# Kernel tuning notes

Measured on AMD Instinct MI355X. Metric: run time of the kernel, lower is better.

The kernel has to match this reference:

```python
import jax, jax.numpy as jnp
import numpy as np

B, F, NQ, DT, TS, K = 16384, 256, 2048, 256, 16, 8
GH, SH, CALH = 128, 128, 16
SPD = DT + TS
SPH = max(int(SPD * 0.25), 16)
CD = DT + 3 + TS + 3  # h_base + y_base + 3 gate stats + z_top + |d_safe| + |d_spec| = 278
CH = max(int(CD * 0.25), 16)
RES_SCALE = 0.1


def _ln(x, g, b):
    m = x.mean(-1, keepdims=True)
    v = ((x - m) ** 2).mean(-1, keepdims=True)
    return (x - m) * jax.lax.rsqrt(v + 1e-5) * g + b


def _resmlp(x, lg, lb, w1, b1, w2, b2):
    h = jnp.maximum(_ln(x, lg, lb) @ w1 + b1, 0.0)
    return h @ w2 + b2


def setup_inputs() -> dict:
    key = jax.random.key(0)
    ks = iter(jax.random.split(key, 48))
    def nrm(shape, s=0.05):
        return jax.random.normal(next(ks), shape, jnp.float32) * s
    d = {}
    d["x_num"] = jax.random.normal(next(ks), (B, F), jnp.float32)
    d["robust_center"] = nrm((1, F), 0.1)
    d["robust_scale"] = jax.random.uniform(next(ks), (1, F), jnp.float32, 0.5, 1.5)
    d["quantile_sorted"] = jnp.sort(jax.random.normal(next(ks), (NQ, F), jnp.float32), axis=0)
    d["stem_w1"] = nrm((3, CALH)); d["stem_b1"] = jnp.zeros((CALH,))
    d["stem_w2"] = nrm((CALH, CALH)); d["stem_b2"] = jnp.zeros((CALH,))
    d["stem_w3"] = nrm((CALH, 1)); d["stem_b3"] = jnp.zeros((1,))
    d["gate_w1"] = nrm((F, GH)); d["gate_b1"] = jnp.zeros((GH,))
    d["gate_w2"] = nrm((GH, F)); d["gate_b2"] = jnp.zeros((F,))
    d["bb_w"] = nrm((F, DT)); d["bb_b"] = jnp.zeros((DT,))
    d["base_w"] = nrm((DT, 1)); d["base_b"] = jnp.zeros((1,))
    d["safe_lg"] = jnp.ones((DT,)); d["safe_lb"] = jnp.zeros((DT,))
    d["safe_w1"] = nrm((DT, SH)); d["safe_b1"] = jnp.zeros((SH,))
    d["safe_w2"] = nrm((SH, 1)); d["safe_b2"] = jnp.zeros((1,))
    d["top_w1"] = nrm((1, TS)); d["top_b1"] = jnp.zeros((TS,))
    d["top_w2"] = nrm((TS, TS)); d["top_b2"] = jnp.zeros((TS,))
    d["spec_lg"] = jnp.ones((SPD,)); d["spec_lb"] = jnp.zeros((SPD,))
    d["spec_w1"] = nrm((SPD, SPH)); d["spec_b1"] = jnp.zeros((SPH,))
    d["spec_w2"] = nrm((SPH, 1)); d["spec_b2"] = jnp.zeros((1,))
    d["conf_lg"] = jnp.ones((CD,)); d["conf_lb"] = jnp.zeros((CD,))
    d["conf_w1"] = nrm((CD, CH)); d["conf_b1"] = jnp.zeros((CH,))
    d["conf_w2"] = nrm((CH, 1)); d["conf_b2"] = jnp.full((1,), -2.0)  # gamma_init_bias
    return d


def _forward(x_num, robust_center, robust_scale, quantile_sorted,
             stem_w1, stem_b1, stem_w2, stem_b2, stem_w3, stem_b3,
             gate_w1, gate_b1, gate_w2, gate_b2,
             bb_w, bb_b, base_w, base_b,
             safe_lg, safe_lb, safe_w1, safe_b1, safe_w2, safe_b2,
             top_w1, top_b1, top_w2, top_b2,
             spec_lg, spec_lb, spec_w1, spec_b1, spec_w2, spec_b2,
             conf_lg, conf_lb, conf_w1, conf_b1, conf_w2, conf_b2):
    # --- calibration views ---
    x_robust = (x_num - robust_center) / robust_scale
    ranks = jax.vmap(jnp.searchsorted, in_axes=(1, 1), out_axes=1)(
        jax.lax.stop_gradient(quantile_sorted), jax.lax.stop_gradient(x_num))  # [B,F] int
    x_quant = jnp.clip(ranks.astype(jnp.float32) / (NQ - 1.0), 0.0, 1.0)
    x_views = jnp.stack([x_num, x_robust, x_quant], axis=-1)  # [B,F,3]
    h = jnp.maximum(x_views @ stem_w1 + stem_b1, 0.0)
    h = jnp.maximum(h @ stem_w2 + stem_b2, 0.0)
    resid = jnp.tanh((h @ stem_w3 + stem_b3)[..., 0])
    x_cal = x_num + RES_SCALE * resid
    # --- input gate ---
    g = jax.nn.sigmoid(jnp.maximum(x_cal @ gate_w1 + gate_b1, 0.0) @ gate_w2 + gate_b2)
    x_gated = x_cal * g
    # --- backbone (stand-in for TMLPBackbone.encode_hidden) ---
    h_base = jnp.maximum(x_gated @ bb_w + bb_b, 0.0)  # [B,DT]
    y_base = h_base @ base_w + base_b  # [B,1]
    gate_mean = g.mean(axis=1, keepdims=True)
    gate_max = g.max(axis=1, keepdims=True)
    gate_std = g.std(axis=1, keepdims=True)  # ddof=0, matches unbiased=False
    delta_safe = _resmlp(h_base, safe_lg, safe_lb, safe_w1, safe_b1, safe_w2, safe_b2)
    # --- top-k feature gather ---
    topk_g, topk_idx = jax.lax.top_k(g, K)
    topk_x = jnp.take_along_axis(x_cal, topk_idx, axis=1)
    topk_w = topk_g / (topk_g.sum(axis=1, keepdims=True) + 1e-6)
    xw = (topk_x * topk_w)[..., None]  # [B,K,1]
    tok = jnp.maximum(xw @ top_w1 + top_b1, 0.0) @ top_w2 + top_b2  # [B,K,TS]
    z_top = tok.mean(axis=1)  # [B,TS]
    delta_spec = _resmlp(jnp.concatenate([h_base, z_top], axis=1),
                         spec_lg, spec_lb, spec_w1, spec_b1, spec_w2, spec_b2)
    conf_in = jnp.concatenate([h_base, y_base, gate_mean, gate_max, gate_std,
                               z_top, jnp.abs(delta_safe), jnp.abs(delta_spec)], axis=1)
    gamma = jax.nn.sigmoid(_resmlp(conf_in, conf_lg, conf_lb, conf_w1, conf_b1, conf_w2, conf_b2))
    return (y_base + delta_safe + gamma * delta_spec)[:, 0]


def reference(x_num, robust_center, robust_scale, quantile_sorted,
              stem_w1, stem_b1, stem_w2, stem_b2, stem_w3, stem_b3,
              gate_w1, gate_b1, gate_w2, gate_b2,
              bb_w, bb_b, base_w, base_b,
              safe_lg, safe_lb, safe_w1, safe_b1, safe_w2, safe_b2,
              top_w1, top_b1, top_w2, top_b2,
              spec_lg, spec_lb, spec_w1, spec_b1, spec_w2, spec_b2,
              conf_lg, conf_lb, conf_w1, conf_b1, conf_w2, conf_b2):
    return _forward(x_num, robust_center, robust_scale, quantile_sorted,
                    stem_w1, stem_b1, stem_w2, stem_b2, stem_w3, stem_b3,
                    gate_w1, gate_b1, gate_w2, gate_b2,
                    bb_w, bb_b, base_w, base_b,
                    safe_lg, safe_lb, safe_w1, safe_b1, safe_w2, safe_b2,
                    top_w1, top_b1, top_w2, top_b2,
                    spec_lg, spec_lb, spec_w1, spec_b1, spec_w2, spec_b2,
                    conf_lg, conf_lb, conf_w1, conf_b1, conf_w2, conf_b2)
```

## Files before the change

### kernel.cpp

```cpp
#include <hip/hip_runtime.h>
#include <math.h>

static constexpr int B  = 16384;
static constexpr int F  = 256;
static constexpr int NQ = 2048;
static constexpr int TS = 16;
static constexpr int KTOP = 8;
static constexpr int SPD = 272;
static constexpr int SPH = 68;
static constexpr int CD  = 278;
static constexpr int CH  = 69;

typedef __attribute__((ext_vector_type(8))) short bf16x8;
typedef __attribute__((ext_vector_type(4))) float f32x4;
typedef _Float16 f16x2 __attribute__((ext_vector_type(2)));

__device__ inline short f2bf(float f) {
    unsigned u = __builtin_bit_cast(unsigned, f);
    unsigned r = (u + 0x7FFF + ((u >> 16) & 1)) >> 16;
    return (short)r;
}

__device__ inline float fast_tanh(float o) {
    o = fminf(fmaxf(o, -15.0f), 15.0f);
    float e = __expf(2.0f * o);
    return (e - 1.0f) / (e + 1.0f);
}

__device__ inline f16x2 cvt2h(float a, float b) {
    return __builtin_bit_cast(f16x2, __builtin_amdgcn_cvt_pkrtz(a, b));
}

__device__ inline unsigned pack2h(float a, float b) {
    return __builtin_bit_cast(unsigned, __builtin_amdgcn_cvt_pkrtz(a, b));
}

__device__ inline void prep_one(const float* W, short* T, int local,
                                int K, int N, int KP) {
    const int n = local / KP, k = local - n * KP;
    T[local] = (k < K && n < N) ? f2bf(W[k * N + n]) : (short)0;
}

__global__ __launch_bounds__(256) void k_prepall(
    const float* __restrict__ gate_w1, const float* __restrict__ gate_w2,
    const float* __restrict__ bb_w,    const float* __restrict__ safe_w1,
    const float* __restrict__ spec_w1, const float* __restrict__ conf_w1,
    const float* __restrict__ qs,
    const float* __restrict__ stem_w2, const float* __restrict__ stem_w3,
    short* __restrict__ w1t, short* __restrict__ w2t, short* __restrict__ bbt,
    short* __restrict__ sw1t, short* __restrict__ spw1t, short* __restrict__ cfw1t,
    float* __restrict__ qs_t,
    unsigned* __restrict__ w2ph, unsigned* __restrict__ w3ph)
{
    const int idx = blockIdx.x * 256 + threadIdx.x;
    if (idx < 32768)       prep_one(gate_w1, w1t,  idx,           256, 128, 256);
    else if (idx < 65536)  prep_one(gate_w2, w2t,  idx - 32768,   128, 256, 128);
    else if (idx < 131072) prep_one(bb_w,    bbt,  idx - 65536,   256, 256, 256);
    else if (idx < 163840) prep_one(safe_w1, sw1t, idx - 131072,  256, 128, 256);
    else if (idx < 200704) prep_one(spec_w1, spw1t, idx - 163840, 272, 68, 288);
    else if (idx < 237568) prep_one(conf_w1, cfw1t, idx - 200704, 278, 69, 288);
    else if (idx < 761856) {
        const int local = idx - 237568;
        const int f = local >> 11, q = local & 2047;
        qs_t[local] = qs[q * 256 + f];
    }
    else if (idx < 761984) {
        const int l = idx - 761856;
        const int t = l >> 4, j = l & 15;
        w2ph[l] = pack2h(stem_w2[(2 * t) * 16 + j], stem_w2[(2 * t + 1) * 16 + j]);
    }
    else if (idx < 761992) {
        const int u = idx - 761984;
        w3ph[u] = pack2h(stem_w3[2 * u], stem_w3[2 * u + 1]);
    }
}

__global__ __launch_bounds__(256) void k_calib7(
    const float* __restrict__ x_num, const float* __restrict__ center,
    const float* __restrict__ scale, const float* __restrict__ qs,
    const float* __restrict__ qs_t,
    const float* __restrict__ sw1, const float* __restrict__ sb1,
    const unsigned* __restrict__ w2ph, const float* __restrict__ sb2,
    const unsigned* __restrict__ w3ph, const float* __restrict__ sb3,
    float* __restrict__ x_cal)
{
    __shared__ float cq[63 * 256];
    const int tid = threadIdx.x;
    const int f = tid;
#pragma unroll 1
    for (int j = 0; j < 63; ++j)
        cq[j * 256 + tid] = qs[(32 * (j + 1)) * 256 + tid];
    __syncthreads();

    const float c = center[f];
    const float inv_sc = 1.0f / scale[f];
    const float* colp = qs_t + (long)f * NQ;
    const long row_base = (long)blockIdx.x * 32;

    float xb[8];
#pragma unroll
    for (int i = 0; i < 8; ++i) xb[i] = x_num[(row_base + i) * F + f];

#pragma unroll 1
    for (int grp = 0; grp < 4; ++grp) {
        const long r0 = row_base + grp * 8;
        float x[8], xr[8];
#pragma unroll
        for (int i = 0; i < 8; ++i) x[i] = xb[i];
        if (grp < 3) {
#pragma unroll
            for (int i = 0; i < 8; ++i) xb[i] = x_num[(r0 + 8 + i) * F + f];
        }
#pragma unroll
        for (int i = 0; i < 8; ++i) xr[i] = (x[i] - c) * inv_sc;

        int lo[8], hi[8];
#pragma unroll
        for (int i = 0; i < 8; ++i) { lo[i] = 0; hi[i] = 63; }
#pragma unroll
        for (int it = 0; it < 6; ++it) {
            float qv[8]; int mid[8];
#pragma unroll
            for (int i = 0; i < 8; ++i) {
                mid[i] = (lo[i] + hi[i]) >> 1;
                qv[i] = cq[mid[i] * 256 + f];
            }
#pragma unroll
            for (int i = 0; i < 8; ++i) {
                if (qv[i] < x[i]) lo[i] = mid[i] + 1; else hi[i] = mid[i];
            }
        }
        int base[8];
        {
            float pm[8];
#pragma unroll
            for (int i = 0; i < 8; ++i) pm[i] = colp[lo[i] * 32 + 16];
#pragma unroll
            for (int i = 0; i < 8; ++i)
                base[i] = lo[i] * 32 + ((pm[i] < x[i]) ? 16 : 0);
        }
        float xq[8];
#pragma unroll
        for (int i = 0; i < 8; ++i) {
            const float4* wp = reinterpret_cast<const float4*>(&colp[base[i]]);
            const float4 a = wp[0], b = wp[1], d = wp[2], e = wp[3];
            int cN = 0;
            cN += (a.x < x[i]); cN += (a.y < x[i]); cN += (a.z < x[i]); cN += (a.w < x[i]);
            cN += (b.x < x[i]); cN += (b.y < x[i]); cN += (b.z < x[i]); cN += (b.w < x[i]);
            cN += (d.x < x[i]); cN += (d.y < x[i]); cN += (d.z < x[i]); cN += (d.w < x[i]);
            cN += (e.x < x[i]); cN += (e.y < x[i]); cN += (e.z < x[i]); cN += (e.w < x[i]);
            const int rank = base[i] + cN;
            xq[i] = fminf((float)rank * (1.0f / (float)(NQ - 1)), 1.0f);
        }

#pragma unroll
        for (int hgrp = 0; hgrp < 2; ++hgrp) {
            const int o4 = hgrp * 4;
            float h2[4][16];
#pragma unroll
            for (int j = 0; j < 16; ++j) {
                const float bb = sb2[j];
#pragma unroll
                for (int i = 0; i < 4; ++i) h2[i][j] = bb;
            }
#pragma unroll 4
            for (int t = 0; t < 8; ++t) {
                const float w0a = sw1[2 * t],     w1a = sw1[16 + 2 * t],     w2a = sw1[32 + 2 * t];
                const float w0b = sw1[2 * t + 1], w1b = sw1[16 + 2 * t + 1], w2b = sw1[32 + 2 * t + 1];
                const float ba = sb1[2 * t], bbv = sb1[2 * t + 1];
                f16x2 hp[4];
#pragma unroll
                for (int i = 0; i < 4; ++i) {
                    const float ha = fmaxf(ba  + x[o4 + i] * w0a + xr[o4 + i] * w1a + xq[o4 + i] * w2a, 0.0f);
                    const float hb = fmaxf(bbv + x[o4 + i] * w0b + xr[o4 + i] * w1b + xq[o4 + i] * w2b, 0.0f);
                    hp[i] = cvt2h(ha, hb);
                }
                unsigned ww[16];
                const uint4* wr = reinterpret_cast<const uint4*>(&w2ph[t * 16]);
                *reinterpret_cast<uint4*>(&ww[0])  = wr[0];
                *reinterpret_cast<uint4*>(&ww[4])  = wr[1];
                *reinterpret_cast<uint4*>(&ww[8])  = wr[2];
                *reinterpret_cast<uint4*>(&ww[12]) = wr[3];
#pragma unroll
                for (int j = 0; j < 16; ++j) {
                    const f16x2 wj = __builtin_bit_cast(f16x2, ww[j]);
#pragma unroll
                    for (int i = 0; i < 4; ++i)
                        h2[i][j] = __builtin_amdgcn_fdot2(hp[i], wj, h2[i][j], false);
                }
            }
            const float b3 = sb3[0];
            float o[4] = {b3, b3, b3, b3};
#pragma unroll
            for (int u = 0; u < 8; ++u) {
                const f16x2 wu = __builtin_bit_cast(f16x2, w3ph[u]);
#pragma unroll
                for (int i = 0; i < 4; ++i) {
                    const f16x2 hh = cvt2h(
                        fmaxf(h2[i][2 * u], 0.0f), fmaxf(h2[i][2 * u + 1], 0.0f));
                    o[i] = __builtin_amdgcn_fdot2(hh, wu, o[i], false);
                }
            }
#pragma unroll
            for (int i = 0; i < 4; ++i)
                x_cal[(r0 + o4 + i) * F + f] = x[o4 + i] + 0.1f * fast_tanh(o[i]);
        }
    }
}

static constexpr int ST1 = 136;
static constexpr int ST2 = 264;

__global__ __launch_bounds__(256) void k_fused(
    const float* __restrict__ x_cal,
    const short* __restrict__ w1t, const float* __restrict__ gate_b1,
    const short* __restrict__ w2t, const float* __restrict__ gate_b2,
    const short* __restrict__ bbt, const float* __restrict__ bb_b,
    float* __restrict__ g, float* __restrict__ h_b)
{
    __shared__ short s_c1[32 * ST1];
    __shared__ short s_xg[32 * ST2];

    const int tid = threadIdx.x;
    const int wave = tid >> 6, lane = tid & 63;
    const int sub = lane & 15, quad = lane >> 4;
    const int wm = wave & 1, wn = wave >> 1;
    const long row0 = (long)blockIdx.x * 32;
    const long mrow = row0 + wm * 16 + sub;

    {
        f32x4 acc[4];
#pragma unroll
        for (int t = 0; t < 4; ++t) acc[t] = (f32x4){0, 0, 0, 0};
#pragma unroll
        for (int k0 = 0; k0 < 256; k0 += 32) {
            const float* ap = x_cal + mrow * 256 + k0 + quad * 8;
            float av[8];
            *reinterpret_cast<float4*>(&av[0]) = *reinterpret_cast<const float4*>(ap);
            *reinterpret_cast<float4*>(&av[4]) = *reinterpret_cast<const float4*>(ap + 4);
            bf16x8 af;
#pragma unroll
            for (int j = 0; j < 8; ++j) af[j] = f2bf(av[j]);
#pragma unroll
            for (int t = 0; t < 4; ++t) {
                const int col = wn * 64 + t * 16 + sub;
                const bf16x8 bf = *reinterpret_cast<const bf16x8*>(
                    &w1t[(long)col * 256 + k0 + quad * 8]);
                acc[t] = __builtin_amdgcn_mfma_f32_16x16x32_bf16(af, bf, acc[t], 0, 0, 0);
            }
        }
#pragma unroll
        for (int t = 0; t < 4; ++t) {
            const int col = wn * 64 + t * 16 + sub;
            const float bb = gate_b1[col];
#pragma unroll
            for (int r = 0; r < 4; ++r) {
                const int rowl = wm * 16 + quad * 4 + r;
                s_c1[rowl * ST1 + col] = f2bf(fmaxf(acc[t][r] + bb, 0.0f));
            }
        }
    }
    __syncthreads();

    {
        f32x4 acc[8];
#pragma unroll
        for (int t = 0; t < 8; ++t) acc[t] = (f32x4){0, 0, 0, 0};
#pragma unroll
        for (int k0 = 0; k0 < 128; k0 += 32) {
            const bf16x8 af = *reinterpret_cast<const bf16x8*>(
                &s_c1[(wm * 16 + sub) * ST1 + k0 + quad * 8]);
#pragma unroll
            for (int t = 0; t < 8; ++t) {
                const int col = wn * 128 + t * 16 + sub;
                const bf16x8 bf = *reinterpret_cast<const bf16x8*>(
                    &w2t[(long)col * 128 + k0 + quad * 8]);
                acc[t] = __builtin_amdgcn_mfma_f32_16x16x32_bf16(af, bf, acc[t], 0, 0, 0);
            }
        }
#pragma unroll
        for (int t = 0; t < 8; ++t) {
            const int col = wn * 128 + t * 16 + sub;
            const float bb = gate_b2[col];
#pragma unroll
            for (int r = 0; r < 4; ++r) {
                const int rowl = wm * 16 + quad * 4 + r;
                const float gv = 1.0f / (1.0f + __expf(-(acc[t][r] + bb)));
                g[(row0 + rowl) * 256 + col] = gv;
                const float xg = x_cal[(row0 + rowl) * 256 + col] * gv;
                s_xg[rowl * ST2 + col] = f2bf(xg);
            }
        }
    }
    __syncthreads();

    {
        f32x4 acc[8];
#pragma unroll
        for (int t = 0; t < 8; ++t) acc[t] = (f32x4){0, 0, 0, 0};
#pragma unroll
        for (int k0 = 0; k0 < 256; k0 += 32) {
            const bf16x8 af = *reinterpret_cast<const bf16x8*>(
                &s_xg[(wm * 16 + sub) * ST2 + k0 + quad * 8]);
#pragma unroll
            for (int t = 0; t < 8; ++t) {
                const int col = wn * 128 + t * 16 + sub;
                const bf16x8 bf = *reinterpret_cast<const bf16x8*>(
                    &bbt[(long)col * 256 + k0 + quad * 8]);
                acc[t] = __builtin_amdgcn_mfma_f32_16x16x32_bf16(af, bf, acc[t], 0, 0, 0);
            }
        }
#pragma unroll
        for (int t = 0; t < 8; ++t) {
            const int col = wn * 128 + t * 16 + sub;
            const float bb = bb_b[col];
#pragma unroll
            for (int r = 0; r < 4; ++r) {
                const int rowl = wm * 16 + quad * 4 + r;
                h_b[(row0 + rowl) * 256 + col] = fmaxf(acc[t][r] + bb, 0.0f);
            }
        }
    }
}

__global__ __launch_bounds__(64) void k_topk(
    const float* __restrict__ g, const float* __restrict__ x_cal,
    const float* __restrict__ tw1, const float* __restrict__ tb1,
    const float* __restrict__ tw2, const float* __restrict__ tb2,
    float* __restrict__ z_top, float* __restrict__ stats)
{
    __shared__ float s_hm[16];
    const int b = blockIdx.x;
    const int lane = threadIdx.x;
    const long base = (long)b * F;

    float gv[4];
#pragma unroll
    for (int i = 0; i < 4; ++i) gv[i] = g[base + lane + 64 * i];

    float s = gv[0] + gv[1] + gv[2] + gv[3];
    float mx = fmaxf(fmaxf(gv[0], gv[1]), fmaxf(gv[2], gv[3]));
    for (int m = 32; m; m >>= 1) {
        s  += __shfl_xor(s, m);
        mx  = fmaxf(mx, __shfl_xor(mx, m));
    }
    const float mean = s * (1.0f / 256.0f);
    float vs = 0.0f;
#pragma unroll
    for (int i = 0; i < 4; ++i) { float d = gv[i] - mean; vs += d * d; }
    for (int m = 32; m; m >>= 1) vs += __shfl_xor(vs, m);
    const float stdv = sqrtf(vs * (1.0f / 256.0f));

    float cur[4]; int curi[4];
#pragma unroll
    for (int i = 0; i < 4; ++i) { cur[i] = gv[i]; curi[i] = lane + 64 * i; }
    float tv[KTOP]; int ti[KTOP]; float vsum = 0.0f;
    for (int r = 0; r < KTOP; ++r) {
        float bv = cur[0]; int bi = curi[0];
#pragma unroll
        for (int i = 1; i < 4; ++i)
            if (cur[i] > bv || (cur[i] == bv && curi[i] < bi)) { bv = cur[i]; bi = curi[i]; }
        for (int m = 32; m; m >>= 1) {
            float ov = __shfl_xor(bv, m);
            int   oi = __shfl_xor(bi, m);
            if (ov > bv || (ov == bv && oi < bi)) { bv = ov; bi = oi; }
        }
        tv[r] = bv; ti[r] = bi; vsum += bv;
#pragma unroll
        for (int i = 0; i < 4; ++i) if (curi[i] == bi) cur[i] = -INFINITY;
    }
    const float denom = 1.0f / (vsum + 1e-6f);

    if (lane < 16) {
        float hm = 0.0f;
        for (int k = 0; k < KTOP; ++k) {
            const float xk = x_cal[base + ti[k]];
            const float xw = xk * (tv[k] * denom);
            hm += fmaxf(xw * tw1[lane] + tb1[lane], 0.0f);
        }
        s_hm[lane] = hm * (1.0f / (float)KTOP);
    }
    __syncthreads();
    if (lane < 16) {
        float z = tb2[lane];
#pragma unroll
        for (int j = 0; j < 16; ++j) z += s_hm[j] * tw2[j * 16 + lane];
        z_top[(long)b * TS + lane] = z;
    }
    if (lane == 0) {
        stats[(long)b * 4 + 0] = mean;
        stats[(long)b * 4 + 1] = mx;
        stats[(long)b * 4 + 2] = stdv;
    }
}

static constexpr int HST = 260;
static constexpr int AST = 312;

template<int KP>
__device__ __forceinline__ void head_mfma16(
    const short* sa, const short* __restrict__ Wt,
    const float* __restrict__ b1v, const float* __restrict__ w2v, int Nreal,
    float (*s_red)[16], int wave, int sub, int quad)
{
    f32x4 acc[2];
#pragma unroll
    for (int t = 0; t < 2; ++t) acc[t] = (f32x4){0, 0, 0, 0};
#pragma unroll
    for (int k0 = 0; k0 < KP; k0 += 32) {
        const bf16x8 af = *reinterpret_cast<const bf16x8*>(
            &sa[sub * AST + k0 + quad * 8]);
#pragma unroll
        for (int t = 0; t < 2; ++t) {
            const int col = wave * 32 + t * 16 + sub;
            const bf16x8 bf = *reinterpret_cast<const bf16x8*>(
                &Wt[(long)col * KP + k0 + quad * 8]);
            acc[t] = __builtin_amdgcn_mfma_f32_16x16x32_bf16(af, bf, acc[t], 0, 0, 0);
        }
    }
    float rsum[4] = {0, 0, 0, 0};
#pragma unroll
    for (int t = 0; t < 2; ++t) {
        const int col = wave * 32 + t * 16 + sub;
        const float bb = (col < Nreal) ? b1v[col] : 0.0f;
        const float ww = (col < Nreal) ? w2v[col] : 0.0f;
#pragma unroll
        for (int rr = 0; rr < 4; ++rr)
            rsum[rr] += fmaxf(acc[t][rr] + bb, 0.0f) * ww;
    }
#pragma unroll
    for (int rr = 0; rr < 4; ++rr)
        for (int m = 1; m < 16; m <<= 1) rsum[rr] += __shfl_xor(rsum[rr], m);
    if (sub == 0) {
#pragma unroll
        for (int rr = 0; rr < 4; ++rr)
            s_red[wave][quad * 4 + rr] = rsum[rr];
    }
}

__global__ __launch_bounds__(256) void k_tail3(
    const float* __restrict__ h_base, const float* __restrict__ z_top,
    const float* __restrict__ gstats,
    const float* __restrict__ base_w, const float* __restrict__ base_b,
    const float* __restrict__ safe_lg, const float* __restrict__ safe_lb,
    const short* __restrict__ sw1t, const float* __restrict__ safe_b1,
    const float* __restrict__ safe_w2, const float* __restrict__ safe_b2,
    const float* __restrict__ spec_lg, const float* __restrict__ spec_lb,
    const short* __restrict__ spw1t, const float* __restrict__ spec_b1,
    const float* __restrict__ spec_w2, const float* __restrict__ spec_b2,
    const float* __restrict__ conf_lg, const float* __restrict__ conf_lb,
    const short* __restrict__ cfw1t, const float* __restrict__ conf_b1,
    const float* __restrict__ conf_w2, const float* __restrict__ conf_b2,
    float* __restrict__ out)
{
    __shared__ float s_h[16 * HST];
    __shared__ short s_a[16 * AST];
    __shared__ float s_z[16 * 16];
    __shared__ float s_g[16 * 4];
    __shared__ float s_sc[16 * 14];
    __shared__ float s_red[4][16];

    const int tid = threadIdx.x;
    const int wave = tid >> 6, lane = tid & 63;
    const int sub = lane & 15, quad = lane >> 4;
    const long row0 = (long)blockIdx.x * 16;

    for (int idx = tid; idx < 16 * 64; idx += 256) {
        const int r = idx >> 6, q = idx & 63;
        *reinterpret_cast<float4*>(&s_h[r * HST + q * 4]) =
            *reinterpret_cast<const float4*>(&h_base[(row0 + r) * 256 + q * 4]);
    }
    if (tid < 256) s_z[tid] = z_top[row0 * 16 + tid];
    if (tid < 64) s_g[tid] = gstats[row0 * 4 + tid];
    __syncthreads();

    {
        const int r = tid >> 4, l16 = tid & 15;
        float S = 0.0f, SS = 0.0f, Y = 0.0f;
#pragma unroll
        for (int i = 0; i < 16; ++i) {
            const int k = l16 + 16 * i;
            const float v = s_h[r * HST + k];
            S += v; SS += v * v; Y += v * base_w[k];
        }
        const float z0 = s_z[r * 16 + l16];
        float Sz = z0, SSz = z0 * z0;
#pragma unroll
        for (int m = 1; m < 16; m <<= 1) {
            S += __shfl_xor(S, m); SS += __shfl_xor(SS, m); Y += __shfl_xor(Y, m);
            Sz += __shfl_xor(Sz, m); SSz += __shfl_xor(SSz, m);
        }
        if (l16 == 0) {
            float* sc = &s_sc[r * 14];
            sc[0] = S; sc[1] = SS; sc[2] = Sz; sc[3] = SSz;
            sc[4] = Y + base_b[0];
            const float mu = S * (1.0f / 256.0f);
            sc[5] = mu;
            sc[6] = rsqrtf(SS * (1.0f / 256.0f) - mu * mu + 1e-5f);
            const float musp = (S + Sz) * (1.0f / (float)SPD);
            sc[7] = musp;
            sc[8] = rsqrtf((SS + SSz) * (1.0f / (float)SPD) - musp * musp + 1e-5f);
        }
    }
    __syncthreads();

    for (int idx = tid; idx < 16 * 128; idx += 256) {
        const int r = idx >> 7, k = (idx & 127) * 2;
        const float mu = s_sc[r * 14 + 5], rs = s_sc[r * 14 + 6];
        const float v0 = (s_h[r * HST + k] - mu) * rs * safe_lg[k] + safe_lb[k];
        const float v1 = (s_h[r * HST + k + 1] - mu) * rs * safe_lg[k + 1] + safe_lb[k + 1];
        const unsigned pk = (unsigned)(unsigned short)f2bf(v0) |
                            ((unsigned)(unsigned short)f2bf(v1) << 16);
        *reinterpret_cast<unsigned*>(&s_a[r * AST + k]) = pk;
    }
    __syncthreads();

    head_mfma16<256>(s_a, sw1t, safe_b1, safe_w2, 128, s_red, wave, sub, quad);
    __syncthreads();

    if (tid < 16)
        s_sc[tid * 14 + 9] = s_red[0][tid] + s_red[1][tid] + s_red[2][tid] + s_red[3][tid] + safe_b2[0];
    for (int idx = tid; idx < 16 * 144; idx += 256) {
        const int r = idx / 144, k = (idx - r * 144) * 2;
        const float mu = s_sc[r * 14 + 7], rs = s_sc[r * 14 + 8];
        float vv[2];
#pragma unroll
        for (int h = 0; h < 2; ++h) {
            const int kk = k + h;
            float raw = (kk < 256) ? s_h[r * HST + kk]
                       : (kk < SPD) ? s_z[r * 16 + kk - 256] : 0.0f;
            vv[h] = (kk < SPD) ? (raw - mu) * rs * spec_lg[kk] + spec_lb[kk] : 0.0f;
        }
        const unsigned pk = (unsigned)(unsigned short)f2bf(vv[0]) |
                            ((unsigned)(unsigned short)f2bf(vv[1]) << 16);
        *reinterpret_cast<unsigned*>(&s_a[r * AST + k]) = pk;
    }
    __syncthreads();

    head_mfma16<288>(s_a, spw1t, spec_b1, spec_w2, SPH, s_red, wave, sub, quad);
    __syncthreads();

    if (tid < 16) {
        float* sc = &s_sc[tid * 14];
        const float dsp = s_red[0][tid] + s_red[1][tid] + s_red[2][tid] + s_red[3][tid] + spec_b2[0];
        sc[10] = dsp;
        const float yb = sc[4];
        const float gm = s_g[tid * 4 + 0], gx = s_g[tid * 4 + 1], gs = s_g[tid * 4 + 2];
        const float ads = fabsf(sc[9]), adp = fabsf(dsp);
        const float es = yb + gm + gx + gs + ads + adp;
        const float eq = yb * yb + gm * gm + gx * gx + gs * gs + ads * ads + adp * adp;
        const float muc = (sc[0] + sc[2] + es) * (1.0f / (float)CD);
        sc[11] = muc;
        sc[12] = rsqrtf((sc[1] + sc[3] + eq) * (1.0f / (float)CD) - muc * muc + 1e-5f);
    }
    __syncthreads();

    for (int idx = tid; idx < 16 * 144; idx += 256) {
        const int r = idx / 144, k = (idx - r * 144) * 2;
        const float mu = s_sc[r * 14 + 11], rs = s_sc[r * 14 + 12];
        float vv[2];
#pragma unroll
        for (int h = 0; h < 2; ++h) {
            const int kk = k + h;
            float raw;
            if (kk < 256)       raw = s_h[r * HST + kk];
            else if (kk == 256) raw = s_sc[r * 14 + 4];
            else if (kk == 257) raw = s_g[r * 4 + 0];
            else if (kk == 258) raw = s_g[r * 4 + 1];
            else if (kk == 259) raw = s_g[r * 4 + 2];
            else if (kk < 276)  raw = s_z[r * 16 + kk - 260];
            else if (kk == 276) raw = fabsf(s_sc[r * 14 + 9]);
            else if (kk == 277) raw = fabsf(s_sc[r * 14 + 10]);
            else                raw = 0.0f;
            vv[h] = (kk < CD) ? (raw - mu) * rs * conf_lg[kk] + conf_lb[kk] : 0.0f;
        }
        const unsigned pk = (unsigned)(unsigned short)f2bf(vv[0]) |
                            ((unsigned)(unsigned short)f2bf(vv[1]) << 16);
        *reinterpret_cast<unsigned*>(&s_a[r * AST + k]) = pk;
    }
    __syncthreads();

    head_mfma16<288>(s_a, cfw1t, conf_b1, conf_w2, CH, s_red, wave, sub, quad);
    __syncthreads();

    if (tid < 16) {
        const float* sc = &s_sc[tid * 14];
        const float gamma = 1.0f / (1.0f + __expf(
            -(s_red[0][tid] + s_red[1][tid] + s_red[2][tid] + s_red[3][tid] + conf_b2[0])));
        out[row0 + tid] = sc[4] + sc[9] + gamma * sc[10];
    }
}

extern "C" void kernel_launch(void* const* d_in, const int* in_sizes, int n_in,
                              void* d_out, int out_size, void* d_ws, size_t ws_size,
                              hipStream_t stream)
{
    const float* x_num   = (const float*)d_in[0];
    const float* center  = (const float*)d_in[1];
    const float* scale   = (const float*)d_in[2];
    const float* qs      = (const float*)d_in[3];
    const float* stem_w1 = (const float*)d_in[4];
    const float* stem_b1 = (const float*)d_in[5];
    const float* stem_w2 = (const float*)d_in[6];
    const float* stem_b2 = (const float*)d_in[7];
    const float* stem_w3 = (const float*)d_in[8];
    const float* stem_b3 = (const float*)d_in[9];
    const float* gate_w1 = (const float*)d_in[10];
    const float* gate_b1 = (const float*)d_in[11];
    const float* gate_w2 = (const float*)d_in[12];
    const float* gate_b2 = (const float*)d_in[13];
    const float* bb_w    = (const float*)d_in[14];
    const float* bb_b    = (const float*)d_in[15];
    const float* base_w  = (const float*)d_in[16];
    const float* base_b  = (const float*)d_in[17];
    const float* safe_lg = (const float*)d_in[18];
    const float* safe_lb = (const float*)d_in[19];
    const float* safe_w1 = (const float*)d_in[20];
    const float* safe_b1 = (const float*)d_in[21];
    const float* safe_w2 = (const float*)d_in[22];
    const float* safe_b2 = (const float*)d_in[23];
    const float* top_w1  = (const float*)d_in[24];
    const float* top_b1  = (const float*)d_in[25];
    const float* top_w2  = (const float*)d_in[26];
    const float* top_b2  = (const float*)d_in[27];
    const float* spec_lg = (const float*)d_in[28];
    const float* spec_lb = (const float*)d_in[29];
    const float* spec_w1 = (const float*)d_in[30];
    const float* spec_b1 = (const float*)d_in[31];
    const float* spec_w2 = (const float*)d_in[32];
    const float* spec_b2 = (const float*)d_in[33];
    const float* conf_lg = (const float*)d_in[34];
    const float* conf_lb = (const float*)d_in[35];
    const float* conf_w1 = (const float*)d_in[36];
    const float* conf_b1 = (const float*)d_in[37];
    const float* conf_w2 = (const float*)d_in[38];
    const float* conf_b2 = (const float*)d_in[39];

    float* ws    = (float*)d_ws;
    float* x_cal = ws;
    float* g_h   = x_cal + (long)B * 256;
    float* g     = g_h   + (long)B * 128;
    float* h_b   = g     + (long)B * 256;
    float* z_top = h_b   + (long)B * 256;
    float* gstat = z_top + (long)B * 16;
    short* w1t   = (short*)(gstat + (long)B * 4);
    short* w2t   = w1t   + 128 * 256;
    short* bbt   = w2t   + 256 * 128;
    short* sw1t  = bbt   + 256 * 256;
    short* spw1t = sw1t  + 128 * 256;
    short* cfw1t = spw1t + 128 * 288;
    unsigned* w2ph = (unsigned*)(cfw1t + 128 * 288);
    unsigned* w3ph = w2ph + 128;
    float* qs_t  = h_b;
    float* out   = (float*)d_out;

    k_prepall<<<2977, 256, 0, stream>>>(gate_w1, gate_w2, bb_w, safe_w1, spec_w1,
                                        conf_w1, qs, stem_w2, stem_w3,
                                        w1t, w2t, bbt, sw1t, spw1t, cfw1t, qs_t,
                                        w2ph, w3ph);
    k_calib7<<<512, 256, 0, stream>>>(x_num, center, scale, qs, qs_t,
                                      stem_w1, stem_b1, w2ph, stem_b2, w3ph, stem_b3,
                                      x_cal);
    k_fused<<<512, 256, 0, stream>>>(x_cal, w1t, gate_b1, w2t, gate_b2, bbt, bb_b,
                                     g, h_b);
    k_topk<<<B, 64, 0, stream>>>(g, x_cal, top_w1, top_b1, top_w2, top_b2, z_top, gstat);
    k_tail3<<<B / 16, 256, 0, stream>>>(h_b, z_top, gstat,
                                        base_w, base_b,
                                        safe_lg, safe_lb, sw1t, safe_b1, safe_w2, safe_b2,
                                        spec_lg, spec_lb, spw1t, spec_b1, spec_w2, spec_b2,
                                        conf_lg, conf_lb, cfw1t, conf_b1, conf_w2, conf_b2,
                                        out);
}
```

Before: 307.8 us.

## Run per-feature calibration stem MLP on MFMA instead of packed fdot2

The per-element 3→16→16→1 calibration MLP is moved from scalar packed-half dot products onto 16x16x32 f16 MFMA instructions. Inputs are staged through a per-wave shared-memory buffer, and hidden activations are redistributed with lane shuffles between the two MFMAs. The final layer is reduced with xor shuffles. Separately, manual bf16 rounding is replaced with the HIP packed float2-to-bf16 conversion in several kernels. Most MFMA lanes carry zero padding, and the extra LDS round trips and shuffles add latency, so the gain over the ALU version is uncertain.

```diff
diff --git a/kernel.cpp b/kernel.cpp
--- a/kernel.cpp
+++ b/kernel.cpp
@@ -1,4 +1,5 @@
 #include <hip/hip_runtime.h>
+#include <hip/hip_bf16.h>
 #include <math.h>
 
 static constexpr int B  = 16384;
@@ -14,6 +15,9 @@
 typedef __attribute__((ext_vector_type(8))) short bf16x8;
 typedef __attribute__((ext_vector_type(4))) float f32x4;
 typedef _Float16 f16x2 __attribute__((ext_vector_type(2)));
+typedef _Float16 f16x8 __attribute__((ext_vector_type(8)));
+typedef unsigned u32x4 __attribute__((ext_vector_type(4)));
+typedef unsigned u32x2 __attribute__((ext_vector_type(2)));
 
 __device__ inline short f2bf(float f) {
     unsigned u = __builtin_bit_cast(unsigned, f);
@@ -21,14 +25,17 @@
     return (short)r;
 }
 
+__device__ inline unsigned pkbf(float a, float b) {
+    __hip_bfloat162 h = __float22bfloat162_rn(make_float2(a, b));
+    unsigned u;
+    __builtin_memcpy(&u, &h, 4);
+    return u;
+}
+
 __device__ inline float fast_tanh(float o) {
     o = fminf(fmaxf(o, -15.0f), 15.0f);
     float e = __expf(2.0f * o);
     return (e - 1.0f) / (e + 1.0f);
-}
-
-__device__ inline f16x2 cvt2h(float a, float b) {
-    return __builtin_bit_cast(f16x2, __builtin_amdgcn_cvt_pkrtz(a, b));
 }
 
 __device__ inline unsigned pack2h(float a, float b) {
@@ -75,22 +82,52 @@
     }
 }
 
-__global__ __launch_bounds__(256) void k_calib7(
+__global__ __launch_bounds__(256) void k_calib8(
     const float* __restrict__ x_num, const float* __restrict__ center,
     const float* __restrict__ scale, const float* __restrict__ qs,
     const float* __restrict__ qs_t,
     const float* __restrict__ sw1, const float* __restrict__ sb1,
     const unsigned* __restrict__ w2ph, const float* __restrict__ sb2,
-    const unsigned* __restrict__ w3ph, const float* __restrict__ sb3,
+    const float* __restrict__ sw3, const float* __restrict__ sb3,
     float* __restrict__ x_cal)
 {
     __shared__ float cq[63 * 256];
+    __shared__ unsigned s_stg[4][1024];
     const int tid = threadIdx.x;
     const int f = tid;
+    const int lane = tid & 63;
+    const int wv = tid >> 6;
+    const int sub = lane & 15, quad = lane >> 4;
+    unsigned* stg = &s_stg[wv][0];
+
 #pragma unroll 1
     for (int j = 0; j < 63; ++j)
         cq[j * 256 + tid] = qs[(32 * (j + 1)) * 256 + tid];
     __syncthreads();
+
+    u32x4 a1u = {0, 0, 0, 0};
+    if (quad == 0) {
+        a1u[0] = pack2h(sw1[sub], sw1[16 + sub]);
+        a1u[1] = pack2h(sw1[32 + sub], 0.0f);
+    }
+    const f16x8 A1 = __builtin_bit_cast(f16x8, a1u);
+    u32x4 a2u = {0, 0, 0, 0};
+    if (quad < 2) {
+        a2u[0] = w2ph[(quad * 4 + 0) * 16 + sub];
+        a2u[1] = w2ph[(quad * 4 + 1) * 16 + sub];
+        a2u[2] = w2ph[(quad * 4 + 2) * 16 + sub];
+        a2u[3] = w2ph[(quad * 4 + 3) * 16 + sub];
+    }
+    const f16x8 A2 = __builtin_bit_cast(f16x8, a2u);
+    const float b1r0 = sb1[quad * 4 + 0], b1r1 = sb1[quad * 4 + 1];
+    const float b1r2 = sb1[quad * 4 + 2], b1r3 = sb1[quad * 4 + 3];
+    const float b2r0 = sb2[quad * 4 + 0], b2r1 = sb2[quad * 4 + 1];
+    const float b2r2 = sb2[quad * 4 + 2], b2r3 = sb2[quad * 4 + 3];
+    const float w3r0 = sw3[quad * 4 + 0], w3r1 = sw3[quad * 4 + 1];
+    const float w3r2 = sw3[quad * 4 + 2], w3r3 = sw3[quad * 4 + 3];
+    const float b3 = sb3[0];
+    const int srcA = quad * 32 + sub;
+    const int srcB = srcA + 16;
 
     const float c = center[f];
     const float inv_sc = 1.0f / scale[f];
@@ -154,56 +191,50 @@
         }
 
 #pragma unroll
-        for (int hgrp = 0; hgrp < 2; ++hgrp) {
-            const int o4 = hgrp * 4;
-            float h2[4][16];
-#pragma unroll
-            for (int j = 0; j < 16; ++j) {
-                const float bb = sb2[j];
-#pragma unroll
-                for (int i = 0; i < 4; ++i) h2[i][j] = bb;
-            }
+        for (int i = 0; i < 8; ++i) {
+            const unsigned plo = pack2h(x[i], xr[i]);
+            const unsigned phi = pack2h(xq[i], 0.0f);
+            *reinterpret_cast<u32x2*>(&stg[(i * 64 + lane) * 2]) = (u32x2){plo, phi};
+        }
+        asm volatile("s_waitcnt lgkmcnt(0)" ::: "memory");
+        __builtin_amdgcn_sched_barrier(0);
+
 #pragma unroll 4
-            for (int t = 0; t < 8; ++t) {
-                const float w0a = sw1[2 * t],     w1a = sw1[16 + 2 * t],     w2a = sw1[32 + 2 * t];
-                const float w0b = sw1[2 * t + 1], w1b = sw1[16 + 2 * t + 1], w2b = sw1[32 + 2 * t + 1];
-                const float ba = sb1[2 * t], bbv = sb1[2 * t + 1];
-                f16x2 hp[4];
-#pragma unroll
-                for (int i = 0; i < 4; ++i) {
-                    const float ha = fmaxf(ba  + x[o4 + i] * w0a + xr[o4 + i] * w1a + xq[o4 + i] * w2a, 0.0f);
-                    const float hb = fmaxf(bbv + x[o4 + i] * w0b + xr[o4 + i] * w1b + xq[o4 + i] * w2b, 0.0f);
-                    hp[i] = cvt2h(ha, hb);
-                }
-                unsigned ww[16];
-                const uint4* wr = reinterpret_cast<const uint4*>(&w2ph[t * 16]);
-                *reinterpret_cast<uint4*>(&ww[0])  = wr[0];
-                *reinterpret_cast<uint4*>(&ww[4])  = wr[1];
-                *reinterpret_cast<uint4*>(&ww[8])  = wr[2];
-                *reinterpret_cast<uint4*>(&ww[12]) = wr[3];
-#pragma unroll
-                for (int j = 0; j < 16; ++j) {
-                    const f16x2 wj = __builtin_bit_cast(f16x2, ww[j]);
-#pragma unroll
-                    for (int i = 0; i < 4; ++i)
-                        h2[i][j] = __builtin_amdgcn_fdot2(hp[i], wj, h2[i][j], false);
-                }
-            }
-            const float b3 = sb3[0];
-            float o[4] = {b3, b3, b3, b3};
-#pragma unroll
-            for (int u = 0; u < 8; ++u) {
-                const f16x2 wu = __builtin_bit_cast(f16x2, w3ph[u]);
-#pragma unroll
-                for (int i = 0; i < 4; ++i) {
-                    const f16x2 hh = cvt2h(
-                        fmaxf(h2[i][2 * u], 0.0f), fmaxf(h2[i][2 * u + 1], 0.0f));
-                    o[i] = __builtin_amdgcn_fdot2(hh, wu, o[i], false);
-                }
-            }
-#pragma unroll
-            for (int i = 0; i < 4; ++i)
-                x_cal[(r0 + o4 + i) * F + f] = x[o4 + i] + 0.1f * fast_tanh(o[i]);
+        for (int t = 0; t < 32; ++t) {
+            u32x4 b1u = {0, 0, 0, 0};
+            if (quad == 0) {
+                const u32x2 v = *reinterpret_cast<const u32x2*>(&stg[(16 * t + sub) * 2]);
+                b1u[0] = v[0]; b1u[1] = v[1];
+            }
+            const f16x8 B1 = __builtin_bit_cast(f16x8, b1u);
+            const f32x4 D1 = __builtin_amdgcn_mfma_f32_16x16x32_f16(
+                A1, B1, (f32x4){0, 0, 0, 0}, 0, 0, 0);
+            const unsigned hlo = pack2h(fmaxf(D1[0] + b1r0, 0.0f), fmaxf(D1[1] + b1r1, 0.0f));
+            const unsigned hhi = pack2h(fmaxf(D1[2] + b1r2, 0.0f), fmaxf(D1[3] + b1r3, 0.0f));
+            unsigned g0 = (unsigned)__shfl((int)hlo, srcA);
+            unsigned g1 = (unsigned)__shfl((int)hhi, srcA);
+            unsigned g2 = (unsigned)__shfl((int)hlo, srcB);
+            unsigned g3 = (unsigned)__shfl((int)hhi, srcB);
+            if (quad >= 2) { g0 = 0; g1 = 0; g2 = 0; g3 = 0; }
+            const f16x8 B2 = __builtin_bit_cast(f16x8, (u32x4){g0, g1, g2, g3});
+            const f32x4 D2 = __builtin_amdgcn_mfma_f32_16x16x32_f16(
+                A2, B2, (f32x4){0, 0, 0, 0}, 0, 0, 0);
+            float p = fmaxf(D2[0] + b2r0, 0.0f) * w3r0
+                    + fmaxf(D2[1] + b2r1, 0.0f) * w3r1
+                    + fmaxf(D2[2] + b2r2, 0.0f) * w3r2
+                    + fmaxf(D2[3] + b2r3, 0.0f) * w3r3;
+            p += __shfl_xor(p, 16);
+            p += __shfl_xor(p, 32);
+            if (quad == 0)
+                reinterpret_cast<float*>(stg)[(16 * t + sub) * 2] = p;
+        }
+        asm volatile("s_waitcnt lgkmcnt(0)" ::: "memory");
+        __builtin_amdgcn_sched_barrier(0);
+
+#pragma unroll
+        for (int i = 0; i < 8; ++i) {
+            const float p = reinterpret_cast<const float*>(stg)[(i * 64 + lane) * 2];
+            x_cal[(r0 + i) * F + f] = x[i] + 0.1f * fast_tanh(p + b3);
         }
     }
 }
@@ -238,9 +269,12 @@
             float av[8];
             *reinterpret_cast<float4*>(&av[0]) = *reinterpret_cast<const float4*>(ap);
             *reinterpret_cast<float4*>(&av[4]) = *reinterpret_cast<const float4*>(ap + 4);
-            bf16x8 af;
-#pragma unroll
-            for (int j = 0; j < 8; ++j) af[j] = f2bf(av[j]);
+            u32x4 afu;
+            afu[0] = pkbf(av[0], av[1]);
+            afu[1] = pkbf(av[2], av[3]);
+            afu[2] = pkbf(av[4], av[5]);
+            afu[3] = pkbf(av[6], av[7]);
+            const bf16x8 af = __builtin_bit_cast(bf16x8, afu);
 #pragma unroll
             for (int t = 0; t < 4; ++t) {
                 const int col = wn * 64 + t * 16 + sub;
@@ -509,9 +543,7 @@
         const float mu = s_sc[r * 14 + 5], rs = s_sc[r * 14 + 6];
         const float v0 = (s_h[r * HST + k] - mu) * rs * safe_lg[k] + safe_lb[k];
         const float v1 = (s_h[r * HST + k + 1] - mu) * rs * safe_lg[k + 1] + safe_lb[k + 1];
-        const unsigned pk = (unsigned)(unsigned short)f2bf(v0) |
-                            ((unsigned)(unsigned short)f2bf(v1) << 16);
-        *reinterpret_cast<unsigned*>(&s_a[r * AST + k]) = pk;
+        *reinterpret_cast<unsigned*>(&s_a[r * AST + k]) = pkbf(v0, v1);
     }
     __syncthreads();
 
@@ -531,9 +563,7 @@
                        : (kk < SPD) ? s_z[r * 16 + kk - 256] : 0.0f;
             vv[h] = (kk < SPD) ? (raw - mu) * rs * spec_lg[kk] + spec_lb[kk] : 0.0f;
         }
-        const unsigned pk = (unsigned)(unsigned short)f2bf(vv[0]) |
-                            ((unsigned)(unsigned short)f2bf(vv[1]) << 16);
-        *reinterpret_cast<unsigned*>(&s_a[r * AST + k]) = pk;
+        *reinterpret_cast<unsigned*>(&s_a[r * AST + k]) = pkbf(vv[0], vv[1]);
     }
     __syncthreads();
 
@@ -574,9 +604,7 @@
             else                raw = 0.0f;
             vv[h] = (kk < CD) ? (raw - mu) * rs * conf_lg[kk] + conf_lb[kk] : 0.0f;
         }
-        const unsigned pk = (unsigned)(unsigned short)f2bf(vv[0]) |
-                            ((unsigned)(unsigned short)f2bf(vv[1]) << 16);
-        *reinterpret_cast<unsigned*>(&s_a[r * AST + k]) = pk;
+        *reinterpret_cast<unsigned*>(&s_a[r * AST + k]) = pkbf(vv[0], vv[1]);
     }
     __syncthreads();
 
@@ -658,8 +686,8 @@
                                         conf_w1, qs, stem_w2, stem_w3,
                                         w1t, w2t, bbt, sw1t, spw1t, cfw1t, qs_t,
                                         w2ph, w3ph);
-    k_calib7<<<512, 256, 0, stream>>>(x_num, center, scale, qs, qs_t,
-                                      stem_w1, stem_b1, w2ph, stem_b2, w3ph, stem_b3,
+    k_calib8<<<512, 256, 0, stream>>>(x_num, center, scale, qs, qs_t,
+                                      stem_w1, stem_b1, w2ph, stem_b2, stem_w3, stem_b3,
                                       x_cal);
     k_fused<<<512, 256, 0, stream>>>(x_cal, w1t, gate_b1, w2t, gate_b2, bbt, bb_b,
                                      g, h_b);
```

Measured after the change: 311.3 us. No clear change (+1.1%).

## Replace binary search with 4-ary search, widen row batch, use packed bf16 converts

Applied to the files above, without the earlier changes.

The calibration kernel swaps the 6-step binary search over 63 coarse quantiles for a 4-ary search: three register-held pivots, then two rounds of three LDS probes each. It also processes 16 rows per pass instead of 8 and batches the LDS fill in groups of 9 loads. Separately, manual bf16 rounding is replaced by the packed __float22bfloat162_rn conversion in the GEMM and tail kernels. The aim is to shorten the dependent LDS-load chain and cut conversion instructions, at the cost of more register pressure from the 16-row arrays.

```diff
diff --git a/kernel.cpp b/kernel.cpp
--- a/kernel.cpp
+++ b/kernel.cpp
@@ -1,4 +1,5 @@
 #include <hip/hip_runtime.h>
+#include <hip/hip_bf16.h>
 #include <math.h>
 
 static constexpr int B  = 16384;
@@ -14,11 +15,19 @@
 typedef __attribute__((ext_vector_type(8))) short bf16x8;
 typedef __attribute__((ext_vector_type(4))) float f32x4;
 typedef _Float16 f16x2 __attribute__((ext_vector_type(2)));
+typedef unsigned u32x4 __attribute__((ext_vector_type(4)));
 
 __device__ inline short f2bf(float f) {
     unsigned u = __builtin_bit_cast(unsigned, f);
     unsigned r = (u + 0x7FFF + ((u >> 16) & 1)) >> 16;
     return (short)r;
+}
+
+__device__ inline unsigned pkbf(float a, float b) {
+    __hip_bfloat162 h = __float22bfloat162_rn(make_float2(a, b));
+    unsigned u;
+    __builtin_memcpy(&u, &h, 4);
+    return u;
 }
 
 __device__ inline float fast_tanh(float o) {
@@ -75,7 +84,7 @@
     }
 }
 
-__global__ __launch_bounds__(256) void k_calib7(
+__global__ __launch_bounds__(256) void k_calib9(
     const float* __restrict__ x_num, const float* __restrict__ center,
     const float* __restrict__ scale, const float* __restrict__ qs,
     const float* __restrict__ qs_t,
@@ -88,8 +97,13 @@
     const int tid = threadIdx.x;
     const int f = tid;
 #pragma unroll 1
-    for (int j = 0; j < 63; ++j)
-        cq[j * 256 + tid] = qs[(32 * (j + 1)) * 256 + tid];
+    for (int j0 = 0; j0 < 63; j0 += 9) {
+        float t[9];
+#pragma unroll
+        for (int u = 0; u < 9; ++u) t[u] = qs[(32 * (j0 + u + 1)) * 256 + tid];
+#pragma unroll
+        for (int u = 0; u < 9; ++u) cq[(j0 + u) * 256 + tid] = t[u];
+    }
     __syncthreads();
 
     const float c = center[f];
@@ -97,51 +111,66 @@
     const float* colp = qs_t + (long)f * NQ;
     const long row_base = (long)blockIdx.x * 32;
 
-    float xb[8];
-#pragma unroll
-    for (int i = 0; i < 8; ++i) xb[i] = x_num[(row_base + i) * F + f];
+    const float cA = cq[15 * 256 + f];
+    const float cB = cq[31 * 256 + f];
+    const float cC = cq[47 * 256 + f];
+
+    float xb[16];
+#pragma unroll
+    for (int i = 0; i < 16; ++i) xb[i] = x_num[(row_base + i) * F + f];
 
 #pragma unroll 1
-    for (int grp = 0; grp < 4; ++grp) {
-        const long r0 = row_base + grp * 8;
-        float x[8], xr[8];
-#pragma unroll
-        for (int i = 0; i < 8; ++i) x[i] = xb[i];
-        if (grp < 3) {
-#pragma unroll
-            for (int i = 0; i < 8; ++i) xb[i] = x_num[(r0 + 8 + i) * F + f];
-        }
-#pragma unroll
-        for (int i = 0; i < 8; ++i) xr[i] = (x[i] - c) * inv_sc;
-
-        int lo[8], hi[8];
-#pragma unroll
-        for (int i = 0; i < 8; ++i) { lo[i] = 0; hi[i] = 63; }
-#pragma unroll
-        for (int it = 0; it < 6; ++it) {
-            float qv[8]; int mid[8];
-#pragma unroll
-            for (int i = 0; i < 8; ++i) {
-                mid[i] = (lo[i] + hi[i]) >> 1;
-                qv[i] = cq[mid[i] * 256 + f];
-            }
-#pragma unroll
-            for (int i = 0; i < 8; ++i) {
-                if (qv[i] < x[i]) lo[i] = mid[i] + 1; else hi[i] = mid[i];
-            }
-        }
-        int base[8];
+    for (int half = 0; half < 2; ++half) {
+        const long r0 = row_base + half * 16;
+        float x[16], xr[16], xq[16];
+#pragma unroll
+        for (int i = 0; i < 16; ++i) x[i] = xb[i];
+        if (half == 0) {
+#pragma unroll
+            for (int i = 0; i < 16; ++i) xb[i] = x_num[(r0 + 16 + i) * F + f];
+        }
+#pragma unroll
+        for (int i = 0; i < 16; ++i) xr[i] = (x[i] - c) * inv_sc;
+
+        int lo[16];
+#pragma unroll
+        for (int i = 0; i < 16; ++i)
+            lo[i] = 16 * (((cA < x[i]) ? 1 : 0) + ((cB < x[i]) ? 1 : 0) + ((cC < x[i]) ? 1 : 0));
         {
-            float pm[8];
-#pragma unroll
-            for (int i = 0; i < 8; ++i) pm[i] = colp[lo[i] * 32 + 16];
-#pragma unroll
-            for (int i = 0; i < 8; ++i)
+            float p1[16], p2[16], p3[16];
+#pragma unroll
+            for (int i = 0; i < 16; ++i) {
+                p1[i] = cq[(lo[i] + 3) * 256 + f];
+                p2[i] = cq[(lo[i] + 7) * 256 + f];
+                p3[i] = cq[(lo[i] + 11) * 256 + f];
+            }
+#pragma unroll
+            for (int i = 0; i < 16; ++i)
+                lo[i] += 4 * (((p1[i] < x[i]) ? 1 : 0) + ((p2[i] < x[i]) ? 1 : 0) + ((p3[i] < x[i]) ? 1 : 0));
+        }
+        {
+            float p1[16], p2[16], p3[16];
+#pragma unroll
+            for (int i = 0; i < 16; ++i) {
+                p1[i] = cq[lo[i] * 256 + f];
+                p2[i] = cq[(lo[i] + 1) * 256 + f];
+                p3[i] = cq[(lo[i] + 2) * 256 + f];
+            }
+#pragma unroll
+            for (int i = 0; i < 16; ++i)
+                lo[i] += ((p1[i] < x[i]) ? 1 : 0) + ((p2[i] < x[i]) ? 1 : 0) + ((p3[i] < x[i]) ? 1 : 0);
+        }
+        int base[16];
+        {
+            float pm[16];
+#pragma unroll
+            for (int i = 0; i < 16; ++i) pm[i] = colp[lo[i] * 32 + 16];
+#pragma unroll
+            for (int i = 0; i < 16; ++i)
                 base[i] = lo[i] * 32 + ((pm[i] < x[i]) ? 16 : 0);
         }
-        float xq[8];
-#pragma unroll
-        for (int i = 0; i < 8; ++i) {
+#pragma unroll
+        for (int i = 0; i < 16; ++i) {
             const float4* wp = reinterpret_cast<const float4*>(&colp[base[i]]);
             const float4 a = wp[0], b = wp[1], d = wp[2], e = wp[3];
             int cN = 0;
@@ -153,8 +182,8 @@
             xq[i] = fminf((float)rank * (1.0f / (float)(NQ - 1)), 1.0f);
         }
 
-#pragma unroll
-        for (int hgrp = 0; hgrp < 2; ++hgrp) {
+#pragma unroll 1
+        for (int hgrp = 0; hgrp < 4; ++hgrp) {
             const int o4 = hgrp * 4;
             float h2[4][16];
 #pragma unroll
@@ -238,9 +267,12 @@
             float av[8];
             *reinterpret_cast<float4*>(&av[0]) = *reinterpret_cast<const float4*>(ap);
             *reinterpret_cast<float4*>(&av[4]) = *reinterpret_cast<const float4*>(ap + 4);
-            bf16x8 af;
-#pragma unroll
-            for (int j = 0; j < 8; ++j) af[j] = f2bf(av[j]);
+            u32x4 afu;
+            afu[0] = pkbf(av[0], av[1]);
+            afu[1] = pkbf(av[2], av[3]);
+            afu[2] = pkbf(av[4], av[5]);
+            afu[3] = pkbf(av[6], av[7]);
+            const bf16x8 af = __builtin_bit_cast(bf16x8, afu);
 #pragma unroll
             for (int t = 0; t < 4; ++t) {
                 const int col = wn * 64 + t * 16 + sub;
@@ -509,9 +541,7 @@
         const float mu = s_sc[r * 14 + 5], rs = s_sc[r * 14 + 6];
         const float v0 = (s_h[r * HST + k] - mu) * rs * safe_lg[k] + safe_lb[k];
         const float v1 = (s_h[r * HST + k + 1] - mu) * rs * safe_lg[k + 1] + safe_lb[k + 1];
-        const unsigned pk = (unsigned)(unsigned short)f2bf(v0) |
-                            ((unsigned)(unsigned short)f2bf(v1) << 16);
-        *reinterpret_cast<unsigned*>(&s_a[r * AST + k]) = pk;
+        *reinterpret_cast<unsigned*>(&s_a[r * AST + k]) = pkbf(v0, v1);
     }
     __syncthreads();
 
@@ -531,9 +561,7 @@
                        : (kk < SPD) ? s_z[r * 16 + kk - 256] : 0.0f;
             vv[h] = (kk < SPD) ? (raw - mu) * rs * spec_lg[kk] + spec_lb[kk] : 0.0f;
         }
-        const unsigned pk = (unsigned)(unsigned short)f2bf(vv[0]) |
-                            ((unsigned)(unsigned short)f2bf(vv[1]) << 16);
-        *reinterpret_cast<unsigned*>(&s_a[r * AST + k]) = pk;
+        *reinterpret_cast<unsigned*>(&s_a[r * AST + k]) = pkbf(vv[0], vv[1]);
     }
     __syncthreads();
 
@@ -574,9 +602,7 @@
             else                raw = 0.0f;
             vv[h] = (kk < CD) ? (raw - mu) * rs * conf_lg[kk] + conf_lb[kk] : 0.0f;
         }
-        const unsigned pk = (unsigned)(unsigned short)f2bf(vv[0]) |
-                            ((unsigned)(unsigned short)f2bf(vv[1]) << 16);
-        *reinterpret_cast<unsigned*>(&s_a[r * AST + k]) = pk;
+        *reinterpret_cast<unsigned*>(&s_a[r * AST + k]) = pkbf(vv[0], vv[1]);
     }
     __syncthreads();
 
@@ -658,7 +684,7 @@
                                         conf_w1, qs, stem_w2, stem_w3,
                                         w1t, w2t, bbt, sw1t, spw1t, cfw1t, qs_t,
                                         w2ph, w3ph);
-    k_calib7<<<512, 256, 0, stream>>>(x_num, center, scale, qs, qs_t,
+    k_calib9<<<512, 256, 0, stream>>>(x_num, center, scale, qs, qs_t,
                                       stem_w1, stem_b1, w2ph, stem_b2, w3ph, stem_b3,
                                       x_cal);
     k_fused<<<512, 256, 0, stream>>>(x_cal, w1t, gate_b1, w2t, gate_b2, bbt, bb_b,
```

Measured after the change: 341.9 us. 1.11x slower.
